# Kernel tuning notes

Measured on AMD Instinct MI355X. Metric: run time of the kernel, lower is better.

## Reference

```python
import jax, jax.numpy as jnp
import numpy as np

B, T, D = 1, 2048, 2048
H, HD = 32, 64
HEAD_COUNTS = np.array([8, 6, 4, 4, 6, 4])  # reasoning, creativity, curiosity, emotional, memory, meta
NEG = -1e9


def rope_tables(seq_len, dim, dtype):
    inv_freq = 1.0 / (10000.0 ** (jnp.arange(0, dim, 2, dtype=jnp.float32) / dim))
    t = jnp.arange(seq_len, dtype=jnp.float32)
    freqs = jnp.outer(t, inv_freq)            # [T, dim/2]
    emb = jnp.concatenate([freqs, freqs], -1) # [T, dim]
    return jnp.cos(emb).astype(dtype), jnp.sin(emb).astype(dtype)


def rotate_half(x):
    x1, x2 = jnp.split(x, 2, axis=-1)
    return jnp.concatenate([-x2, x1], axis=-1)


def setup_inputs() -> dict:
    key = jax.random.key(0)
    ks = jax.random.split(key, 8)
    x = jax.random.normal(ks[0], (B, T, D), jnp.float32)
    mask = jnp.tril(jnp.ones((T, T), jnp.int32))[None, None]  # causal [1,1,T,T]
    context_bias = jax.random.normal(ks[1], (B, T, T), jnp.float32) * 0.02
    mod_weights = jax.random.uniform(ks[2], (B, 6), jnp.float32, 0.5, 1.5)
    Wq = jax.random.normal(ks[3], (D, D), jnp.float32) * 0.02
    Wk = jax.random.normal(ks[4], (D, D), jnp.float32) * 0.02
    Wv = jax.random.normal(ks[5], (D, D), jnp.float32) * 0.02
    Wo = jax.random.normal(ks[6], (D, D), jnp.float32) * 0.02
    temp_scales = jnp.ones((H,), jnp.float32)
    return {"x": x, "mask": mask, "context_bias": context_bias,
            "mod_weights": mod_weights, "Wq": Wq, "Wk": Wk, "Wv": Wv,
            "Wo": Wo, "temp_scales": temp_scales}


def reference(x, mask, context_bias, mod_weights, Wq, Wk, Wv, Wo, temp_scales):
    b, t, d = x.shape
    # projections (torch Linear: y = x @ W.T)
    Q = (x @ Wq.T).reshape(b, t, H, HD).transpose(0, 2, 1, 3)  # [B,H,T,HD]
    K = (x @ Wk.T).reshape(b, t, H, HD).transpose(0, 2, 1, 3)
    V = (x @ Wv.T).reshape(b, t, H, HD).transpose(0, 2, 1, 3)
    cos, sin = rope_tables(t, HD, x.dtype)
    cos, sin = cos[None, None], sin[None, None]
    Q = Q * cos + rotate_half(Q) * sin
    K = K * cos + rotate_half(K) * sin
    scale = (HD ** -0.5) * temp_scales.reshape(1, H, 1, 1)
    attn = jnp.einsum('bhqd,bhkd->bhqk', Q, K) * scale
    attn = jnp.where(mask == 0, NEG, attn)
    attn = attn + context_bias[:, None]
    # per-head module reweight: expand [B,6] -> [B,H]
    w = jnp.repeat(mod_weights, np.asarray(HEAD_COUNTS), axis=1, total_repeat_length=H)
    attn = attn * w[:, :, None, None]
    attn = jax.nn.softmax(attn, axis=-1)
    out = jnp.einsum('bhqk,bhkd->bhqd', attn, V)
    out = out.transpose(0, 2, 1, 3).reshape(b, t, d)
    return out @ Wo.T
```

## Files before the change

### kernel.cpp

```cpp
#include <hip/hip_runtime.h>
#include <hip/hip_bf16.h>
#include <cstdint>
#include <cstddef>

typedef __bf16 bf16;
typedef bf16 bf16x4 __attribute__((ext_vector_type(4)));
typedef bf16 bf16x8 __attribute__((ext_vector_type(8)));
typedef float f32x4 __attribute__((ext_vector_type(4)));

#define MFMA_BF16(a,b,c) __builtin_amdgcn_mfma_f32_16x16x32_bf16((a),(b),(c),0,0,0)

typedef __attribute__((address_space(1))) const void gvoid;
typedef __attribute__((address_space(3))) void svoid;
__device__ __forceinline__ void gload16(const bf16* g, bf16* l){
  __builtin_amdgcn_global_load_lds((gvoid*)g, (svoid*)l, 16, 0, 0);
}

__device__ __forceinline__ int head_group(int h){
  return (h<8)?0:(h<14)?1:(h<18)?2:(h<22)?3:(h<28)?4:5;
}

struct CvtArgs { const float* src[6]; bf16* dst[6]; };
__global__ __launch_bounds__(256) void cvt6_kernel(CvtArgs a, int n){
  const int z = blockIdx.y;
  const float* __restrict__ in = a.src[z];
  bf16* __restrict__ out = a.dst[z];
  int i = (blockIdx.x*256 + threadIdx.x)*8;
  if (i >= n) return;
  const float4* p = (const float4*)(in + i);
  float4 va = p[0], vb = p[1];
  bf16x8 o;
  o[0]=(bf16)va.x; o[1]=(bf16)va.y; o[2]=(bf16)va.z; o[3]=(bf16)va.w;
  o[4]=(bf16)vb.x; o[5]=(bf16)vb.y; o[6]=(bf16)vb.z; o[7]=(bf16)vb.w;
  *(bf16x8*)(out+i) = o;
}

__global__ __launch_bounds__(256) void rope_tab_kernel(float* __restrict__ cosT,
                                                       float* __restrict__ sinT){
  const int t = blockIdx.x*8 + (threadIdx.x>>5);
  const int i = threadIdx.x&31;
  float invf = powf(10000.0f, -((float)i)/32.0f);
  float ang = (float)t * invf;
  cosT[t*32+i] = cosf(ang);
  sinT[t*32+i] = sinf(ang);
}

__device__ __forceinline__ void gemm_core(const bf16* __restrict__ A,
                                          const bf16* __restrict__ B,
                                          int row0, int col0,
                                          f32x4 (&acc)[4][4]){
  __shared__ bf16 As[128*32];
  __shared__ bf16 Bs[128*32];
  const int tid  = threadIdx.x;
  const int wave = tid>>6, lane = tid&63;
  const int l16  = lane&15, lg = lane>>4;
  const int wr   = wave>>1, wc = wave&1;

  const bf16* Ag0 = A + (size_t)(row0 + wave*32      + (lane>>2))*2048 + (lane&3)*8;
  const bf16* Ag1 = A + (size_t)(row0 + wave*32 + 16 + (lane>>2))*2048 + (lane&3)*8;
  const bf16* Bg0 = B + (size_t)(col0 + wave*32      + (lane>>2))*2048 + (lane&3)*8;
  const bf16* Bg1 = B + (size_t)(col0 + wave*32 + 16 + (lane>>2))*2048 + (lane&3)*8;
  bf16* AsB0 = As + (wave*32     )*32;
  bf16* AsB1 = As + (wave*32 + 16)*32;
  bf16* BsB0 = Bs + (wave*32     )*32;
  bf16* BsB1 = Bs + (wave*32 + 16)*32;

  #pragma unroll
  for (int m=0;m<4;++m)
    #pragma unroll
    for (int n=0;n<4;++n)
      #pragma unroll
      for (int r=0;r<4;++r) acc[m][n][r] = 0.f;

  for (int kt=0; kt<64; ++kt){
    const int ko = kt*32;
    gload16(Ag0 + ko, AsB0);
    gload16(Ag1 + ko, AsB1);
    gload16(Bg0 + ko, BsB0);
    gload16(Bg1 + ko, BsB1);
    __syncthreads();
    bf16x8 af[4], bfr[4];
    #pragma unroll
    for (int m=0;m<4;++m) af[m]  = *(const bf16x8*)&As[(wr*64+m*16+l16)*32 + lg*8];
    #pragma unroll
    for (int n=0;n<4;++n) bfr[n] = *(const bf16x8*)&Bs[(wc*64+n*16+l16)*32 + lg*8];
    #pragma unroll
    for (int m=0;m<4;++m)
      #pragma unroll
      for (int n=0;n<4;++n)
        acc[m][n] = MFMA_BF16(af[m], bfr[n], acc[m][n]);
    __syncthreads();
  }
}

__global__ __launch_bounds__(256) void gemm_qkv_kernel(
    const bf16* __restrict__ A,
    const bf16* __restrict__ B0, const bf16* __restrict__ B1, const bf16* __restrict__ B2,
    bf16* __restrict__ Qs, bf16* __restrict__ Ks, bf16* __restrict__ Vt,
    const float* __restrict__ cosT, const float* __restrict__ sinT,
    const float* __restrict__ mw, const float* __restrict__ ts){
  const int z = blockIdx.z;
  const bf16* B = (z==0)?B0:((z==1)?B1:B2);
  const int row0 = blockIdx.y*128, col0 = blockIdx.x*128;

  f32x4 acc[4][4];
  gemm_core(A, B, row0, col0, acc);

  const int tid  = threadIdx.x;
  const int wave = tid>>6, lane = tid&63;
  const int l16  = lane&15, lg = lane>>4;
  const int wr   = wave>>1, wc = wave&1;
  const int h    = (col0 + wc*64) >> 6;

  if (z == 2){
    #pragma unroll
    for (int n=0;n<4;++n){
      const int d = n*16 + l16;
      #pragma unroll
      for (int m=0;m<4;++m){
        const int t0 = row0 + wr*64 + m*16 + lg*4;
        bf16x4 v;
        #pragma unroll
        for (int r=0;r<4;++r) v[r] = (bf16)acc[m][n][r];
        *(bf16x4*)&Vt[((size_t)h*64 + d)*2048 + t0] = v;
      }
    }
  } else {
    const float sc = (z==0) ? 0.125f*ts[h]*mw[head_group(h)] : 1.0f;
    bf16* Out = (z==0) ? Qs : Ks;
    #pragma unroll
    for (int m=0;m<4;++m){
      #pragma unroll
      for (int r=0;r<4;++r){
        const int t = row0 + wr*64 + m*16 + lg*4 + r;
        const float* ct = cosT + t*32;
        const float* st = sinT + t*32;
        bf16* dst = Out + ((size_t)h*2048 + t)*64;
        #pragma unroll
        for (int n=0;n<2;++n){
          const int i = n*16 + l16;
          const float c = ct[i], s = st[i];
          const float a1 = acc[m][n][r], a2 = acc[m][n+2][r];
          dst[i]    = (bf16)((a1*c - a2*s)*sc);
          dst[i+32] = (bf16)((a2*c + a1*s)*sc);
        }
      }
    }
  }
}

__global__ __launch_bounds__(256) void gemm_out_kernel(
    const bf16* __restrict__ A, const bf16* __restrict__ B, float* __restrict__ C){
  const int row0 = blockIdx.y*128, col0 = blockIdx.x*128;
  f32x4 acc[4][4];
  gemm_core(A, B, row0, col0, acc);
  const int tid  = threadIdx.x;
  const int wave = tid>>6, lane = tid&63;
  const int l16  = lane&15, lg = lane>>4;
  const int wr   = wave>>1, wc = wave&1;
  #pragma unroll
  for (int m=0;m<4;++m)
    #pragma unroll
    for (int n=0;n<4;++n)
      #pragma unroll
      for (int r=0;r<4;++r){
        size_t idx = (size_t)(row0 + wr*64 + m*16 + lg*4 + r)*2048
                   + col0 + wc*64 + n*16 + l16;
        C[idx] = acc[m][n][r];
      }
}

__global__ __launch_bounds__(512) void attn_kernel(
    const bf16* __restrict__ Qs, const bf16* __restrict__ Ks,
    const bf16* __restrict__ Vt, const bf16* __restrict__ biasb,
    const float* __restrict__ mw, bf16* __restrict__ attout){
  const int n  = blockIdx.x;
  const int h  = ((n>>8)<<4) | ((n>>4)&15);
  const int qt = (n&256) ? (n&15) : 15-(n&15);
  const int tid = threadIdx.x, wid = tid>>6, lane = tid&63;
  const int l16 = lane&15, lg = lane>>4;
  const float w_h = mw[head_group(h)];
  const int qbase = qt*128 + wid*16;
  const int qg0 = qbase + lg*4;
  const int qtop = qbase + 15;
  const int nkt = 2*qt + 2;

  __shared__ bf16 Kl[2][4096];
  __shared__ bf16 Vl[2][4096];
  __shared__ bf16 plds[8][16][72];

  const int srow = tid>>3, ssub = tid&7;
  const bf16* Kg = Ks + (size_t)h*2048*64 + srow*64 + ssub*8;
  const bf16* Vg = Vt + ((size_t)h*64 + srow)*2048 + ssub*8;
  const int wsw = srow*64 + ((ssub ^ (srow&7))<<3);

  const bf16* Qp = Qs + ((size_t)h*2048 + qbase + l16)*64 + lg*8;
  bf16x8 qf0 = *(const bf16x8*)Qp;
  bf16x8 qf1 = *(const bf16x8*)(Qp + 32);

  const bf16* Bg = biasb + (size_t)qg0*2048;

  f32x4 O[4];
  float l[4] = {0.f,0.f,0.f,0.f};
  #pragma unroll
  for (int c=0;c<4;++c)
    #pragma unroll
    for (int r=0;r<4;++r) O[c][r] = 0.f;

  int rK0[4], rK1[4];
  #pragma unroll
  for (int c=0;c<4;++c){
    const int row = c*16 + l16;
    rK0[c] = row*64 + (((lg  ) ^ (row&7))<<3);
    rK1[c] = row*64 + (((4+lg) ^ (row&7))<<3);
  }

  float bc[4][4];
  #pragma unroll
  for (int c=0;c<4;++c)
    #pragma unroll
    for (int r=0;r<4;++r)
      bc[c][r] = w_h * (float)Bg[(size_t)r*2048 + c*16 + l16];

  {
    bf16x8 k0v = *(const bf16x8*)Kg;
    bf16x8 v0v = *(const bf16x8*)Vg;
    *(bf16x8*)&Kl[0][wsw] = k0v;
    *(bf16x8*)&Vl[0][wsw] = v0v;
  }
  __syncthreads();

  int cur = 0;
  for (int kt=0; kt<nkt; ++kt){
    const int k0 = kt*64;
    const bool more = (kt+1 < nkt);
    bf16x8 kA, vA;
    float bn[4][4];
    if (more){
      kA = *(const bf16x8*)(Kg + (size_t)(k0+64)*64);
      vA = *(const bf16x8*)(Vg + (k0+64));
      #pragma unroll
      for (int c=0;c<4;++c)
        #pragma unroll
        for (int r=0;r<4;++r)
          bn[c][r] = w_h * (float)Bg[(size_t)r*2048 + (k0+64) + c*16 + l16];
    }

    if (k0 <= qtop){
      f32x4 S[4];
      #pragma unroll
      for (int c=0;c<4;++c)
        #pragma unroll
        for (int r=0;r<4;++r) S[c][r] = bc[c][r];

      __builtin_amdgcn_s_setprio(1);
      #pragma unroll
      for (int c=0;c<4;++c){
        bf16x8 kf0 = *(const bf16x8*)&Kl[cur][rK0[c]];
        bf16x8 kf1 = *(const bf16x8*)&Kl[cur][rK1[c]];
        S[c] = MFMA_BF16(qf0, kf0, S[c]);
        S[c] = MFMA_BF16(qf1, kf1, S[c]);
      }
      __builtin_amdgcn_s_setprio(0);

      #pragma unroll
      for (int c=0;c<4;++c){
        const int kg = k0 + c*16 + l16;
        #pragma unroll
        for (int r=0;r<4;++r){
          float s = S[c][r];
          if (kg > qg0+r) s = -1e30f;
          const float p = __expf(s - 4.0f);
          S[c][r] = p; l[r] += p;
        }
      }

      #pragma unroll
      for (int c=0;c<4;++c)
        #pragma unroll
        for (int r=0;r<4;++r)
          plds[wid][lg*4+r][c*16+l16] = (bf16)S[c][r];
      bf16x8 pf0 = *(const bf16x8*)&plds[wid][l16][lg*8];
      bf16x8 pf1 = *(const bf16x8*)&plds[wid][l16][lg*8+32];

      __builtin_amdgcn_s_setprio(1);
      #pragma unroll
      for (int c=0;c<4;++c){
        bf16x8 vf0 = *(const bf16x8*)&Vl[cur][rK0[c]];
        bf16x8 vf1 = *(const bf16x8*)&Vl[cur][rK1[c]];
        O[c] = MFMA_BF16(pf0, vf0, O[c]);
        O[c] = MFMA_BF16(pf1, vf1, O[c]);
      }
      __builtin_amdgcn_s_setprio(0);
    }

    if (more){
      *(bf16x8*)&Kl[cur^1][wsw] = kA;
      *(bf16x8*)&Vl[cur^1][wsw] = vA;
      #pragma unroll
      for (int c=0;c<4;++c)
        #pragma unroll
        for (int r=0;r<4;++r) bc[c][r] = bn[c][r];
    }
    __syncthreads();
    cur ^= (int)more;
  }

  #pragma unroll
  for (int r=0;r<4;++r){
    float v = l[r];
    v += __shfl_xor(v,1);
    v += __shfl_xor(v,2);
    v += __shfl_xor(v,4);
    v += __shfl_xor(v,8);
    l[r] = 1.0f / v;
  }
  #pragma unroll
  for (int c=0;c<4;++c)
    #pragma unroll
    for (int r=0;r<4;++r)
      attout[(size_t)(qg0+r)*2048 + h*64 + c*16 + l16] = (bf16)(O[c][r]*l[r]);
}

extern "C" void kernel_launch(void* const* d_in, const int* in_sizes, int n_in,
                              void* d_out, int out_size, void* d_ws, size_t ws_size,
                              hipStream_t stream){
  const float* x    = (const float*)d_in[0];
  const float* bias = (const float*)d_in[2];
  const float* mw   = (const float*)d_in[3];
  const float* Wq   = (const float*)d_in[4];
  const float* Wk   = (const float*)d_in[5];
  const float* Wv   = (const float*)d_in[6];
  const float* Wo   = (const float*)d_in[7];
  const float* ts   = (const float*)d_in[8];
  float* out = (float*)d_out;

  const size_t SZ = (size_t)2048*2048;
  bf16* base = (bf16*)d_ws;
  bf16* xb   = base;
  bf16* Wqb  = base + 1*SZ;
  bf16* Wkb  = base + 2*SZ;
  bf16* Wvb  = base + 3*SZ;
  bf16* Wob  = base + 4*SZ;
  bf16* bb   = base + 5*SZ;
  bf16* Qsb  = base + 6*SZ;
  bf16* Ksb  = base + 7*SZ;
  bf16* Vtb  = base + 8*SZ;
  bf16* att  = base + 9*SZ;
  float* cosT = (float*)(base + 10*SZ);
  float* sinT = cosT + 2048*32;

  CvtArgs ca;
  ca.src[0]=x;  ca.src[1]=Wq;  ca.src[2]=Wk;  ca.src[3]=Wv;  ca.src[4]=Wo;  ca.src[5]=bias;
  ca.dst[0]=xb; ca.dst[1]=Wqb; ca.dst[2]=Wkb; ca.dst[3]=Wvb; ca.dst[4]=Wob; ca.dst[5]=bb;
  const int nb = (int)(SZ/8/256);
  cvt6_kernel<<<dim3(nb,6),256,0,stream>>>(ca, (int)SZ);
  rope_tab_kernel<<<256,256,0,stream>>>(cosT, sinT);
  gemm_qkv_kernel<<<dim3(16,16,3),256,0,stream>>>(xb, Wqb,Wkb,Wvb,
                                                  Qsb,Ksb,Vtb, cosT,sinT, mw,ts);
  attn_kernel<<<512,512,0,stream>>>(Qsb,Ksb,Vtb,bb,mw,att);
  gemm_out_kernel<<<dim3(16,16),256,0,stream>>>(att, Wob, out);
}
```

Baseline: 180.4 us.

## Stream K/V tiles straight to LDS with async loads and skip unneeded bias/mask work

Replaces the register-staged K/V tile copies with global_load_lds direct-to-LDS loads. The source addresses are pre-swizzled so the LDS layout stays the same. The constant softmax offset is folded into the preloaded bias, the causal mask is applied only on diagonal tiles, and bias prefetch is skipped for tiles past the causal limit. The aim is to cut register pressure and VGPR round-trips and to drop per-element compare work, at the cost of relying on the wave-uniform LDS base semantics of the direct load.

```diff
diff --git a/kernel.cpp b/kernel.cpp
--- a/kernel.cpp
+++ b/kernel.cpp
@@ -189,10 +189,10 @@
   __shared__ bf16 Vl[2][4096];
   __shared__ bf16 plds[8][16][72];
 
-  const int srow = tid>>3, ssub = tid&7;
-  const bf16* Kg = Ks + (size_t)h*2048*64 + srow*64 + ssub*8;
-  const bf16* Vg = Vt + ((size_t)h*64 + srow)*2048 + ssub*8;
-  const int wsw = srow*64 + ((ssub ^ (srow&7))<<3);
+  const int srow = wid*8 + (lane>>3);
+  const int sswz = ((lane&7) ^ (srow&7))<<3;
+  const bf16* KgS = Ks + (size_t)h*2048*64 + srow*64 + sswz;
+  const bf16* VgS = Vt + ((size_t)h*64 + srow)*2048 + sswz;
 
   const bf16* Qp = Qs + ((size_t)h*2048 + qbase + l16)*64 + lg*8;
   bf16x8 qf0 = *(const bf16x8*)Qp;
@@ -220,30 +220,30 @@
   for (int c=0;c<4;++c)
     #pragma unroll
     for (int r=0;r<4;++r)
-      bc[c][r] = w_h * (float)Bg[(size_t)r*2048 + c*16 + l16];
-
-  {
-    bf16x8 k0v = *(const bf16x8*)Kg;
-    bf16x8 v0v = *(const bf16x8*)Vg;
-    *(bf16x8*)&Kl[0][wsw] = k0v;
-    *(bf16x8*)&Vl[0][wsw] = v0v;
-  }
+      bc[c][r] = w_h * (float)Bg[(size_t)r*2048 + c*16 + l16] - 4.0f;
+
+  gload16(KgS, &Kl[0][wid*512]);
+  gload16(VgS, &Vl[0][wid*512]);
   __syncthreads();
 
   int cur = 0;
   for (int kt=0; kt<nkt; ++kt){
     const int k0 = kt*64;
     const bool more = (kt+1 < nkt);
-    bf16x8 kA, vA;
+    if (more){
+      bf16* kd = cur ? &Kl[0][wid*512] : &Kl[1][wid*512];
+      bf16* vd = cur ? &Vl[0][wid*512] : &Vl[1][wid*512];
+      gload16(KgS + (size_t)(k0+64)*64, kd);
+      gload16(VgS + (k0+64), vd);
+    }
     float bn[4][4];
-    if (more){
-      kA = *(const bf16x8*)(Kg + (size_t)(k0+64)*64);
-      vA = *(const bf16x8*)(Vg + (k0+64));
+    const bool needb = more && (k0+64 <= qtop);
+    if (needb){
       #pragma unroll
       for (int c=0;c<4;++c)
         #pragma unroll
         for (int r=0;r<4;++r)
-          bn[c][r] = w_h * (float)Bg[(size_t)r*2048 + (k0+64) + c*16 + l16];
+          bn[c][r] = w_h * (float)Bg[(size_t)r*2048 + (k0+64) + c*16 + l16] - 4.0f;
     }
 
     if (k0 <= qtop){
@@ -263,16 +263,25 @@
       }
       __builtin_amdgcn_s_setprio(0);
 
-      #pragma unroll
-      for (int c=0;c<4;++c){
-        const int kg = k0 + c*16 + l16;
-        #pragma unroll
-        for (int r=0;r<4;++r){
-          float s = S[c][r];
-          if (kg > qg0+r) s = -1e30f;
-          const float p = __expf(s - 4.0f);
-          S[c][r] = p; l[r] += p;
+      if (k0 + 63 > qbase){
+        #pragma unroll
+        for (int c=0;c<4;++c){
+          const int kg = k0 + c*16 + l16;
+          #pragma unroll
+          for (int r=0;r<4;++r){
+            float p = __expf(S[c][r]);
+            if (kg > qg0+r) p = 0.f;
+            S[c][r] = p; l[r] += p;
+          }
         }
+      } else {
+        #pragma unroll
+        for (int c=0;c<4;++c)
+          #pragma unroll
+          for (int r=0;r<4;++r){
+            const float p = __expf(S[c][r]);
+            S[c][r] = p; l[r] += p;
+          }
       }
 
       #pragma unroll
@@ -294,9 +303,7 @@
       __builtin_amdgcn_s_setprio(0);
     }
 
-    if (more){
-      *(bf16x8*)&Kl[cur^1][wsw] = kA;
-      *(bf16x8*)&Vl[cur^1][wsw] = vA;
+    if (needb){
       #pragma unroll
       for (int c=0;c<4;++c)
         #pragma unroll
```

New measurement: 182.9 us. Within noise of the previous version (+1.4%).

## Replace QKV GEMM with 256x256-tile double-buffered pipelined kernel

Applied to the files above, without the earlier changes.

Replaces the 128x128 single-buffered QKV projection GEMM with a 256x256-tile, 512-thread kernel. It double-buffers LDS over 64-wide K steps, using XOR-swizzled layout and explicit vmcnt/lgkmcnt waits so global-to-LDS loads overlap MFMA work. The larger tile raises operand reuse, but the grid drops to 192 blocks and register pressure rises with 128 accumulators per thread. The RoPE/scale epilogue is unchanged, and the attention kernel only inlines a constant.

```diff
diff --git a/kernel.cpp b/kernel.cpp
--- a/kernel.cpp
+++ b/kernel.cpp
@@ -14,6 +14,16 @@
 typedef __attribute__((address_space(3))) void svoid;
 __device__ __forceinline__ void gload16(const bf16* g, bf16* l){
   __builtin_amdgcn_global_load_lds((gvoid*)g, (svoid*)l, 16, 0, 0);
+}
+
+__device__ __forceinline__ void wait_lgkm0(){
+  asm volatile("s_waitcnt lgkmcnt(0)" ::: "memory");
+  __builtin_amdgcn_sched_barrier(0);
+}
+template<int N> __device__ __forceinline__ void wait_vm(){
+  if constexpr (N==0) asm volatile("s_waitcnt vmcnt(0)" ::: "memory");
+  else                asm volatile("s_waitcnt vmcnt(4)" ::: "memory");
+  __builtin_amdgcn_sched_barrier(0);
 }
 
 __device__ __forceinline__ int head_group(int h){
@@ -45,6 +55,162 @@
   sinT[t*32+i] = sinf(ang);
 }
 
+__global__ __launch_bounds__(512,2) void gemm_qkv256_kernel(
+    const bf16* __restrict__ A,
+    const bf16* __restrict__ B0, const bf16* __restrict__ B1, const bf16* __restrict__ B2,
+    bf16* __restrict__ Qs, bf16* __restrict__ Ks, bf16* __restrict__ Vt,
+    const float* __restrict__ cosT, const float* __restrict__ sinT,
+    const float* __restrict__ mw, const float* __restrict__ ts){
+  const int z = blockIdx.z;
+  const bf16* B = (z==0)?B0:((z==1)?B1:B2);
+  const int row0 = blockIdx.y*256, col0 = blockIdx.x*256;
+
+  __shared__ bf16 lds[2][2][2][8192];
+
+  const int tid = threadIdx.x, w = tid>>6, lane = tid&63;
+  const int l16 = lane&15, lg = lane>>4;
+  const int wr = w>>2, wc = w&3;
+  const int axor = (l16>>1)&3;
+
+  const int grow = w*32 + (lane>>2);
+  const int gcol = ((lane&3) ^ ((lane>>3)&3))*8;
+  const bf16* Ag = A + (size_t)(row0 + grow)*2048 + gcol;
+  const bf16* Bg = B + (size_t)(col0 + grow)*2048 + gcol;
+
+  f32x4 acc[8][4];
+  #pragma unroll
+  for (int m=0;m<8;++m)
+    #pragma unroll
+    for (int nn=0;nn<4;++nn)
+      #pragma unroll
+      for (int r=0;r<4;++r) acc[m][nn][r] = 0.f;
+
+  bf16x8 af[4], bfr[4];
+
+#define STAGE2(MAT, KS, BUF, KT1) \
+  { const bf16* gp = ((MAT)? Bg : Ag) + (size_t)(KT1)*64 + (KS)*32;   \
+    bf16* lp = (bf16*)&lds[BUF][MAT][KS][w*1024];                      \
+    gload16(gp, lp);                                                   \
+    gload16(gp + (size_t)16*2048, lp + 512); }
+
+#define LDB4(KS, CB) \
+  _Pragma("unroll") for (int nn=0;nn<4;++nn) \
+    bfr[nn] = *(const bf16x8*)&lds[CB][1][KS][(wc*64+nn*16+l16)*32 + ((lg^axor)<<3)];
+#define LDA4(MG, KS, CB) \
+  _Pragma("unroll") for (int i=0;i<4;++i) \
+    af[i] = *(const bf16x8*)&lds[CB][0][KS][(wr*128+((MG)*4+i)*16+l16)*32 + ((lg^axor)<<3)];
+#define MFMA16(MG) \
+  __builtin_amdgcn_s_setprio(1); \
+  _Pragma("unroll") for (int i=0;i<4;++i) \
+    _Pragma("unroll") for (int nn=0;nn<4;++nn) \
+      acc[(MG)*4+i][nn] = MFMA_BF16(af[i], bfr[nn], acc[(MG)*4+i][nn]); \
+  __builtin_amdgcn_s_setprio(0);
+
+  STAGE2(0,0,0,0)
+  STAGE2(1,0,0,0)
+  STAGE2(0,1,0,0)
+  STAGE2(1,1,0,0)
+  wait_vm<4>();
+  __builtin_amdgcn_s_barrier();
+
+  for (int kt=0; kt<31; ++kt){
+    const int cb = kt&1, nbuf = cb^1;
+    LDB4(0, cb)
+    LDA4(0, 0, cb)
+    STAGE2(0,0,nbuf,kt+1)
+    __builtin_amdgcn_s_barrier();
+    wait_lgkm0();
+    MFMA16(0)
+    __builtin_amdgcn_s_barrier();
+    LDA4(1, 0, cb)
+    STAGE2(1,0,nbuf,kt+1)
+    __builtin_amdgcn_s_barrier();
+    wait_lgkm0();
+    MFMA16(1)
+    wait_vm<4>();
+    __builtin_amdgcn_s_barrier();
+    LDB4(1, cb)
+    LDA4(0, 1, cb)
+    STAGE2(0,1,nbuf,kt+1)
+    __builtin_amdgcn_s_barrier();
+    wait_lgkm0();
+    MFMA16(0)
+    __builtin_amdgcn_s_barrier();
+    LDA4(1, 1, cb)
+    STAGE2(1,1,nbuf,kt+1)
+    __builtin_amdgcn_s_barrier();
+    wait_lgkm0();
+    MFMA16(1)
+    wait_vm<4>();
+    __builtin_amdgcn_s_barrier();
+  }
+  {
+    const int cb = 1;
+    LDB4(0, cb)
+    LDA4(0, 0, cb)
+    __builtin_amdgcn_s_barrier();
+    wait_lgkm0();
+    MFMA16(0)
+    __builtin_amdgcn_s_barrier();
+    LDA4(1, 0, cb)
+    __builtin_amdgcn_s_barrier();
+    wait_lgkm0();
+    MFMA16(1)
+    wait_vm<0>();
+    __builtin_amdgcn_s_barrier();
+    LDB4(1, cb)
+    LDA4(0, 1, cb)
+    __builtin_amdgcn_s_barrier();
+    wait_lgkm0();
+    MFMA16(0)
+    __builtin_amdgcn_s_barrier();
+    LDA4(1, 1, cb)
+    wait_lgkm0();
+    MFMA16(1)
+  }
+#undef STAGE2
+#undef LDB4
+#undef LDA4
+#undef MFMA16
+
+  const int h = blockIdx.x*4 + wc;
+  if (z == 2){
+    #pragma unroll
+    for (int nn=0;nn<4;++nn){
+      const int d = nn*16 + l16;
+      #pragma unroll
+      for (int m=0;m<8;++m){
+        const int t0 = row0 + wr*128 + m*16 + lg*4;
+        bf16x4 v;
+        #pragma unroll
+        for (int r=0;r<4;++r) v[r] = (bf16)acc[m][nn][r];
+        *(bf16x4*)&Vt[((size_t)h*64 + d)*2048 + t0] = v;
+      }
+    }
+  } else {
+    const float sc = (z==0) ? 0.125f*ts[h]*mw[head_group(h)] : 1.0f;
+    bf16* Out = (z==0) ? Qs : Ks;
+    #pragma unroll
+    for (int m=0;m<8;++m){
+      #pragma unroll
+      for (int r=0;r<4;++r){
+        const int t = row0 + wr*128 + m*16 + lg*4 + r;
+        const float* ct = cosT + t*32;
+        const float* st = sinT + t*32;
+        bf16* dst = Out + ((size_t)h*2048 + t)*64;
+        #pragma unroll
+        for (int nn=0;nn<2;++nn){
+          const int i = nn*16 + l16;
+          const float c = ct[i], s = st[i];
+          const float a1 = acc[m][nn][r], a2 = acc[m][nn+2][r];
+          dst[i]    = (bf16)((a1*c - a2*s)*sc);
+          dst[i+32] = (bf16)((a2*c + a1*s)*sc);
+        }
+      }
+    }
+  }
+}
+
 __device__ __forceinline__ void gemm_core(const bf16* __restrict__ A,
                                           const bf16* __restrict__ B,
                                           int row0, int col0,
@@ -90,62 +256,6 @@
       for (int n=0;n<4;++n)
         acc[m][n] = MFMA_BF16(af[m], bfr[n], acc[m][n]);
     __syncthreads();
-  }
-}
-
-__global__ __launch_bounds__(256) void gemm_qkv_kernel(
-    const bf16* __restrict__ A,
-    const bf16* __restrict__ B0, const bf16* __restrict__ B1, const bf16* __restrict__ B2,
-    bf16* __restrict__ Qs, bf16* __restrict__ Ks, bf16* __restrict__ Vt,
-    const float* __restrict__ cosT, const float* __restrict__ sinT,
-    const float* __restrict__ mw, const float* __restrict__ ts){
-  const int z = blockIdx.z;
-  const bf16* B = (z==0)?B0:((z==1)?B1:B2);
-  const int row0 = blockIdx.y*128, col0 = blockIdx.x*128;
-
-  f32x4 acc[4][4];
-  gemm_core(A, B, row0, col0, acc);
-
-  const int tid  = threadIdx.x;
-  const int wave = tid>>6, lane = tid&63;
-  const int l16  = lane&15, lg = lane>>4;
-  const int wr   = wave>>1, wc = wave&1;
-  const int h    = (col0 + wc*64) >> 6;
-
-  if (z == 2){
-    #pragma unroll
-    for (int n=0;n<4;++n){
-      const int d = n*16 + l16;
-      #pragma unroll
-      for (int m=0;m<4;++m){
-        const int t0 = row0 + wr*64 + m*16 + lg*4;
-        bf16x4 v;
-        #pragma unroll
-        for (int r=0;r<4;++r) v[r] = (bf16)acc[m][n][r];
-        *(bf16x4*)&Vt[((size_t)h*64 + d)*2048 + t0] = v;
-      }
-    }
-  } else {
-    const float sc = (z==0) ? 0.125f*ts[h]*mw[head_group(h)] : 1.0f;
-    bf16* Out = (z==0) ? Qs : Ks;
-    #pragma unroll
-    for (int m=0;m<4;++m){
-      #pragma unroll
-      for (int r=0;r<4;++r){
-        const int t = row0 + wr*64 + m*16 + lg*4 + r;
-        const float* ct = cosT + t*32;
-        const float* st = sinT + t*32;
-        bf16* dst = Out + ((size_t)h*2048 + t)*64;
-        #pragma unroll
-        for (int n=0;n<2;++n){
-          const int i = n*16 + l16;
-          const float c = ct[i], s = st[i];
-          const float a1 = acc[m][n][r], a2 = acc[m][n+2][r];
-          dst[i]    = (bf16)((a1*c - a2*s)*sc);
-          dst[i+32] = (bf16)((a2*c + a1*s)*sc);
-        }
-      }
-    }
   }
 }
 
@@ -182,7 +292,6 @@
   const float w_h = mw[head_group(h)];
   const int qbase = qt*128 + wid*16;
   const int qg0 = qbase + lg*4;
-  const int qtop = qbase + 15;
   const int nkt = 2*qt + 2;
 
   __shared__ bf16 Kl[2][4096];
@@ -246,7 +355,7 @@
           bn[c][r] = w_h * (float)Bg[(size_t)r*2048 + (k0+64) + c*16 + l16];
     }
 
-    if (k0 <= qtop){
+    if (k0 <= qbase + 15){
       f32x4 S[4];
       #pragma unroll
       for (int c=0;c<4;++c)
@@ -356,8 +465,8 @@
   const int nb = (int)(SZ/8/256);
   cvt6_kernel<<<dim3(nb,6),256,0,stream>>>(ca, (int)SZ);
   rope_tab_kernel<<<256,256,0,stream>>>(cosT, sinT);
-  gemm_qkv_kernel<<<dim3(16,16,3),256,0,stream>>>(xb, Wqb,Wkb,Wvb,
-                                                  Qsb,Ksb,Vtb, cosT,sinT, mw,ts);
+  gemm_qkv256_kernel<<<dim3(8,8,3),512,0,stream>>>(xb, Wqb,Wkb,Wvb,
+                                                   Qsb,Ksb,Vtb, cosT,sinT, mw,ts);
   attn_kernel<<<512,512,0,stream>>>(Qsb,Ksb,Vtb,bb,mw,att);
   gemm_out_kernel<<<dim3(16,16),256,0,stream>>>(att, Wob, out);
 }
```

New measurement: 182.0 us. About the same (+0.9%).
